# Optimization experiments

Hardware: AMD Instinct MI355X
Metric: run time of the kernel (lower is better)

Reference implementation:

```python
import jax, jax.numpy as jnp
import numpy as np

B, W = 131072, 32
N_SCEN, SDIM = 19, 16
EMBED_DIM, COMP_DIM = 768, 64
INPUT_DIM = EMBED_DIM + N_SCEN * SDIM  # 1072


def setup_inputs() -> dict:
    key = jax.random.key(0)
    k1, k2, k3, k4, k5, k6 = jax.random.split(key, 6)
    intent_embedding = jax.random.normal(k1, (B, EMBED_DIM), dtype=jnp.float32)
    scenario_ids = jax.random.randint(k2, (B, W), 0, N_SCEN, dtype=jnp.int32)
    # Prefix mask: the torch loop iterates the first int(mask.sum()) slots,
    # so the mask must be a contiguous run of ones.
    lengths = jax.random.randint(k3, (B,), 1, W + 1)
    scenario_mask = (jnp.arange(W)[None, :] < lengths[:, None]).astype(jnp.float32)
    # Parameters (init: normal std=0.01, zero biases)
    scenario_table = 0.01 * jax.random.normal(k4, (N_SCEN, SDIM), dtype=jnp.float32)
    W1 = 0.01 * jax.random.normal(k5, (INPUT_DIM, COMP_DIM), dtype=jnp.float32)
    b1 = jnp.zeros((COMP_DIM,), dtype=jnp.float32)
    W2 = 0.01 * jax.random.normal(k6, (COMP_DIM, 1), dtype=jnp.float32)
    b2 = jnp.zeros((1,), dtype=jnp.float32)
    return {
        "intent_embedding": intent_embedding,
        "scenario_ids": scenario_ids,
        "scenario_mask": scenario_mask,
        "scenario_table": scenario_table,
        "W1": W1, "b1": b1, "W2": W2, "b2": b2,
    }


def reference(intent_embedding, scenario_ids, scenario_mask, scenario_table, W1, b1, W2, b2):
    # Embedding lookup: [B, W, SDIM]
    embeds = scenario_table[scenario_ids]
    masked = embeds * scenario_mask[:, :, None]
    # Vectorized scatter-add into per-scenario bins: [B, N_SCEN, SDIM]
    batch_idx = jnp.arange(scenario_ids.shape[0])[:, None]
    bag3 = jnp.zeros(
        (scenario_ids.shape[0], N_SCEN, SDIM), dtype=embeds.dtype
    ).at[batch_idx, scenario_ids].add(masked)
    counts = scenario_mask.sum(axis=1, keepdims=True)
    bag_vec = bag3.reshape(scenario_ids.shape[0], N_SCEN * SDIM) / jnp.maximum(counts, 1.0)
    combined = jnp.concatenate([intent_embedding, bag_vec], axis=1)  # [B, 1072]
    h = jax.nn.relu(combined @ W1 + b1)  # dropout is identity in eval mode
    return jnp.tanh(h @ W2 + b2)  # [B, 1]
```

## Files before the change

kernel.cpp:

```cpp
#include <hip/hip_runtime.h>
#include <hip/hip_bf16.h>
#include <math.h>

using short8 = __attribute__((ext_vector_type(8))) short;
using f32x4  = __attribute__((ext_vector_type(4))) float;
using fv4    = __attribute__((ext_vector_type(4))) float;

#define EMB 768
#define CD  64
#define NSCEN 19
#define KSTEPS 24
#define NCHUNKS (25 * 4)
#define QB 14336
#define BM 128

__device__ __forceinline__ ushort f2bf(float x) {
    unsigned u = __float_as_uint(x);
    u += 0x7FFFu + ((u >> 16) & 1u);
    return (ushort)(u >> 16);
}

__device__ __forceinline__ uint cvt2(float x, float y) {
    __hip_bfloat162 h = __float22bfloat162_rn(make_float2(x, y));
    union { __hip_bfloat162 h; uint u; } c;
    c.h = h;
    return c.u;
}

__global__ void prep_W1T(const float* __restrict__ table,
                         const float* __restrict__ W1,
                         ushort* __restrict__ W1T) {
    int e0 = (blockIdx.x * 256 + threadIdx.x) * 4;
    if (e0 >= NCHUNKS * 512) return;
    int chunk = e0 >> 9, r = e0 & 511;
    int lane = r >> 3, j0 = r & 7;
    int ks = chunk >> 2, ct = chunk & 3;
    int col = ct * 16 + (lane & 15);
    int kbase = ks * 32 + ((lane >> 4) << 3) + j0;
    ushort res[4];
#pragma unroll
    for (int q = 0; q < 4; ++q) {
        int k = kbase + q;
        float v = 0.f;
        if (k < EMB) {
            v = W1[(size_t)k * CD + col];
        } else {
            int s = k - EMB;
            if (s < NSCEN) {
#pragma unroll
                for (int d = 0; d < 16; ++d)
                    v += table[s * 16 + d] * W1[(size_t)(EMB + s * 16 + d) * CD + col];
            }
        }
        res[q] = f2bf(v);
    }
    *(ushort4*)&W1T[e0] = make_ushort4(res[0], res[1], res[2], res[3]);
}

__global__ __launch_bounds__(512, 4)
void scorer_mfma(const float* __restrict__ emb,
                 const int* __restrict__ ids,
                 const float* __restrict__ mask,
                 const ushort* __restrict__ W1T,
                 const float* __restrict__ b1,
                 const float* __restrict__ W2,
                 const float* __restrict__ b2,
                 float* __restrict__ out) {
    __shared__ __align__(16) ushort Bq[2][QB];
    __shared__ __align__(16) ushort bagb[8][16][32];

    const int t    = threadIdx.x;
    const int w    = t >> 6;
    const int lane = t & 63;
    const int lr   = lane & 15;
    const int lg   = lane >> 4;
    const int row0 = blockIdx.x * BM;

    const int hrow = row0 + w * 16 + lr;
    const int*   idrow = ids  + (size_t)hrow * 32 + lg * 8;
    const float* mrow  = mask + (size_t)hrow * 32 + lg * 8;
    int4   iv0 = ((const int4*)idrow)[0],  iv1 = ((const int4*)idrow)[1];
    float4 mv0 = ((const float4*)mrow)[0], mv1 = ((const float4*)mrow)[1];

    const float* ap = emb + (size_t)(row0 + w * 16 + lr) * EMB + (lg << 3);
    fv4 aA[2], aB[2];
#define LOADA(dst, kks) do {                                   \
    const float* _p = ap + (kks) * 32;                         \
    dst[0] = *(const fv4*)(_p);                                \
    dst[1] = *(const fv4*)(_p + 4);                            \
} while (0)
    LOADA(aA, 0);

    uint4 f0, f1, f2, f3;
#define ISSUE_FILL(qs) do {                                                  \
    const uint* _g = (const uint*)((const char*)W1T + (size_t)(qs) * 4096);  \
    f0 = *(const uint4*)(_g + (t)        * 4);                               \
    f1 = *(const uint4*)(_g + (t + 512)  * 4);                               \
    f2 = *(const uint4*)(_g + (t + 1024) * 4);                               \
    if (t < 256) f3 = *(const uint4*)(_g + (t + 1536) * 4);                  \
} while (0)
#define WRITE_FILL(bufi) do {                                                \
    uint* _l = (uint*)&Bq[bufi][0];                                          \
    *(uint4*)(_l + (t)        * 4) = f0;                                     \
    *(uint4*)(_l + (t + 512)  * 4) = f1;                                     \
    *(uint4*)(_l + (t + 1024) * 4) = f2;                                     \
    if (t < 256) *(uint4*)(_l + (t + 1536) * 4) = f3;                        \
} while (0)
    ISSUE_FILL(0);

    float bin[NSCEN];
#pragma unroll
    for (int s = 0; s < NSCEN; ++s) bin[s] = 0.f;
    float cnt = 0.f;
#define HSLOT(idv, mvv) do {                                   \
    cnt += mvv;                                                \
    _Pragma("unroll")                                          \
    for (int s = 0; s < NSCEN; ++s)                            \
        bin[s] += (idv == s) ? mvv : 0.f;                      \
} while (0)
    HSLOT(iv0.x, mv0.x); HSLOT(iv0.y, mv0.y); HSLOT(iv0.z, mv0.z); HSLOT(iv0.w, mv0.w);
    HSLOT(iv1.x, mv1.x); HSLOT(iv1.y, mv1.y); HSLOT(iv1.z, mv1.z); HSLOT(iv1.w, mv1.w);
#undef HSLOT
    cnt += __shfl_xor(cnt, 16);
    cnt += __shfl_xor(cnt, 32);
#pragma unroll
    for (int s = 0; s < NSCEN; ++s) {
        bin[s] += __shfl_xor(bin[s], 16);
        bin[s] += __shfl_xor(bin[s], 32);
    }
    {
        float rc = 1.0f / fmaxf(cnt, 1.0f);
        if (lane < 16) {
            uint u[16];
#pragma unroll
            for (int p = 0; p < 9; ++p) u[p] = cvt2(bin[2 * p] * rc, bin[2 * p + 1] * rc);
            u[9] = cvt2(bin[18] * rc, 0.f);
#pragma unroll
            for (int p = 10; p < 16; ++p) u[p] = 0u;
            ushort* bp = &bagb[w][lane][0];
#pragma unroll
            for (int q = 0; q < 4; ++q)
                *(uint4*)(bp + q * 8) = make_uint4(u[4 * q], u[4 * q + 1], u[4 * q + 2], u[4 * q + 3]);
        }
    }

    WRITE_FILL(0);
    ISSUE_FILL(6);
    __syncthreads();

    f32x4 acc[4];
#pragma unroll
    for (int j = 0; j < 4; ++j) acc[j] = (f32x4)0.f;

    short8 bqr[4];
#define LDSB(bufi, ksl) do {                                   \
    const ushort* _l = &Bq[bufi][(ksl) * 2048 + lane * 8];     \
    bqr[0] = *(const short8*)(_l);                             \
    bqr[1] = *(const short8*)(_l + 512);                       \
    bqr[2] = *(const short8*)(_l + 1024);                      \
    bqr[3] = *(const short8*)(_l + 1536);                      \
} while (0)

#define STEP(areg) do {                                                     \
    union { uint u[4]; short8 s; } _c;                                      \
    _c.u[0] = cvt2(areg[0][0], areg[0][1]);                                 \
    _c.u[1] = cvt2(areg[0][2], areg[0][3]);                                 \
    _c.u[2] = cvt2(areg[1][0], areg[1][1]);                                 \
    _c.u[3] = cvt2(areg[1][2], areg[1][3]);                                 \
    acc[0] = __builtin_amdgcn_mfma_f32_16x16x32_bf16(_c.s, bqr[0], acc[0], 0, 0, 0); \
    acc[1] = __builtin_amdgcn_mfma_f32_16x16x32_bf16(_c.s, bqr[1], acc[1], 0, 0, 0); \
    acc[2] = __builtin_amdgcn_mfma_f32_16x16x32_bf16(_c.s, bqr[2], acc[2], 0, 0, 0); \
    acc[3] = __builtin_amdgcn_mfma_f32_16x16x32_bf16(_c.s, bqr[3], acc[3], 0, 0, 0); \
} while (0)

#define QUARTER(bufi, qs) do {                                              \
    _Pragma("unroll")                                                       \
    for (int _ksl = 0; _ksl < 6; ++_ksl) {                                  \
        const int _ks = (qs) + _ksl;                                        \
        LDSB(bufi, _ksl);                                                   \
        if ((_ks & 1) == 0) {                                               \
            if (_ks + 1 <= 23) LOADA(aB, _ks + 1);                          \
            STEP(aA);                                                       \
        } else {                                                            \
            if (_ks + 1 <= 23) LOADA(aA, _ks + 1);                          \
            STEP(aB);                                                       \
        }                                                                   \
    }                                                                       \
} while (0)

    WRITE_FILL(1);
    ISSUE_FILL(12);
    QUARTER(0, 0);
    __syncthreads();

    WRITE_FILL(0);
    ISSUE_FILL(18);
    QUARTER(1, 6);
    __syncthreads();

    WRITE_FILL(1);
    QUARTER(0, 12);
    __syncthreads();

    QUARTER(1, 18);
    {
        short8 ab = *(const short8*)&bagb[w][lr][lg << 3];
        LDSB(1, 6);
        acc[0] = __builtin_amdgcn_mfma_f32_16x16x32_bf16(ab, bqr[0], acc[0], 0, 0, 0);
        acc[1] = __builtin_amdgcn_mfma_f32_16x16x32_bf16(ab, bqr[1], acc[1], 0, 0, 0);
        acc[2] = __builtin_amdgcn_mfma_f32_16x16x32_bf16(ab, bqr[2], acc[2], 0, 0, 0);
        acc[3] = __builtin_amdgcn_mfma_f32_16x16x32_bf16(ab, bqr[3], acc[3], 0, 0, 0);
    }

    float b1v[4], w2v[4];
#pragma unroll
    for (int ct = 0; ct < 4; ++ct) {
        int c = ct * 16 + lr;
        b1v[ct] = b1[c];
        w2v[ct] = W2[c];
    }
    const float b2v = b2[0];
#pragma unroll
    for (int r = 0; r < 4; ++r) {
        float p = 0.f;
#pragma unroll
        for (int ct = 0; ct < 4; ++ct) {
            float h = acc[ct][r] + b1v[ct];
            p += fmaxf(h, 0.f) * w2v[ct];
        }
        p += __shfl_xor(p, 1);
        p += __shfl_xor(p, 2);
        p += __shfl_xor(p, 4);
        p += __shfl_xor(p, 8);
        if (lr == 0)
            out[row0 + w * 16 + (lg << 2) + r] = tanhf(p + b2v);
    }
#undef ISSUE_FILL
#undef WRITE_FILL
#undef LOADA
#undef LDSB
#undef STEP
#undef QUARTER
}

extern "C" void kernel_launch(void* const* d_in, const int* in_sizes, int n_in,
                              void* d_out, int out_size, void* d_ws, size_t ws_size,
                              hipStream_t stream) {
    const float* emb   = (const float*)d_in[0];
    const int*   ids   = (const int*)d_in[1];
    const float* mask  = (const float*)d_in[2];
    const float* table = (const float*)d_in[3];
    const float* W1    = (const float*)d_in[4];
    const float* b1    = (const float*)d_in[5];
    const float* W2    = (const float*)d_in[6];
    const float* b2    = (const float*)d_in[7];
    float* out  = (float*)d_out;
    ushort* W1T = (ushort*)d_ws;

    prep_W1T<<<50, 256, 0, stream>>>(table, W1, W1T);
    const int nblocks = out_size / BM;
    scorer_mfma<<<nblocks, 512, 0, stream>>>(emb, ids, mask, W1T, b1, W2, b2, out);
}
```

Baseline: 90.28 us.

## Shrink LDS weight staging to 4-kstep groups and raise occupancy to 6 blocks

```diff
diff --git a/kernel.cpp b/kernel.cpp
--- a/kernel.cpp
+++ b/kernel.cpp
@@ -11,7 +11,7 @@
 #define NSCEN 19
 #define KSTEPS 24
 #define NCHUNKS (25 * 4)
-#define QB 14336
+#define GB 8192
 #define BM 128
 
 __device__ __forceinline__ ushort f2bf(float x) {
@@ -57,7 +57,7 @@
     *(ushort4*)&W1T[e0] = make_ushort4(res[0], res[1], res[2], res[3]);
 }
 
-__global__ __launch_bounds__(512, 4)
+__global__ __launch_bounds__(512, 6)
 void scorer_mfma(const float* __restrict__ emb,
                  const int* __restrict__ ids,
                  const float* __restrict__ mask,
@@ -66,7 +66,8 @@
                  const float* __restrict__ W2,
                  const float* __restrict__ b2,
                  float* __restrict__ out) {
-    __shared__ __align__(16) ushort Bq[2][QB];
+    __shared__ __align__(16) ushort Bq[2][GB];
+    __shared__ __align__(16) ushort Pb[2048];
     __shared__ __align__(16) ushort bagb[8][16][32];
 
     const int t    = threadIdx.x;
@@ -91,22 +92,20 @@
 } while (0)
     LOADA(aA, 0);
 
-    uint4 f0, f1, f2, f3;
-#define ISSUE_FILL(qs) do {                                                  \
-    const uint* _g = (const uint*)((const char*)W1T + (size_t)(qs) * 4096);  \
-    f0 = *(const uint4*)(_g + (t)        * 4);                               \
-    f1 = *(const uint4*)(_g + (t + 512)  * 4);                               \
-    f2 = *(const uint4*)(_g + (t + 1024) * 4);                               \
-    if (t < 256) f3 = *(const uint4*)(_g + (t + 1536) * 4);                  \
+    uint4 fA, fB;
+#define ISSUE_FILL(g) do {                                                    \
+    const uint* _g = (const uint*)((const char*)W1T + (size_t)(g) * 16384);  \
+    fA = *(const uint4*)(_g + (t)       * 4);                                \
+    fB = *(const uint4*)(_g + (t + 512) * 4);                                \
 } while (0)
 #define WRITE_FILL(bufi) do {                                                \
     uint* _l = (uint*)&Bq[bufi][0];                                          \
-    *(uint4*)(_l + (t)        * 4) = f0;                                     \
-    *(uint4*)(_l + (t + 512)  * 4) = f1;                                     \
-    *(uint4*)(_l + (t + 1024) * 4) = f2;                                     \
-    if (t < 256) *(uint4*)(_l + (t + 1536) * 4) = f3;                        \
+    *(uint4*)(_l + (t)       * 4) = fA;                                      \
+    *(uint4*)(_l + (t + 512) * 4) = fB;                                      \
 } while (0)
     ISSUE_FILL(0);
+    uint4 pv;
+    if (t < 256) pv = *(const uint4*)((const char*)W1T + 98304 + t * 16);
 
     float bin[NSCEN];
 #pragma unroll
@@ -145,7 +144,8 @@
     }
 
     WRITE_FILL(0);
-    ISSUE_FILL(6);
+    if (t < 256) *(uint4*)((char*)Pb + t * 16) = pv;
+    ISSUE_FILL(1);
     __syncthreads();
 
     f32x4 acc[4];
@@ -173,9 +173,9 @@
     acc[3] = __builtin_amdgcn_mfma_f32_16x16x32_bf16(_c.s, bqr[3], acc[3], 0, 0, 0); \
 } while (0)
 
-#define QUARTER(bufi, qs) do {                                              \
+#define GROUP(bufi, qs) do {                                                \
     _Pragma("unroll")                                                       \
-    for (int _ksl = 0; _ksl < 6; ++_ksl) {                                  \
+    for (int _ksl = 0; _ksl < 4; ++_ksl) {                                  \
         const int _ks = (qs) + _ksl;                                        \
         LDSB(bufi, _ksl);                                                   \
         if ((_ks & 1) == 0) {                                               \
@@ -188,28 +188,38 @@
     }                                                                       \
 } while (0)
 
+    WRITE_FILL(1); ISSUE_FILL(2);
+    GROUP(0, 0);
+    __syncthreads();
+
+    WRITE_FILL(0); ISSUE_FILL(3);
+    GROUP(1, 4);
+    __syncthreads();
+
+    WRITE_FILL(1); ISSUE_FILL(4);
+    GROUP(0, 8);
+    __syncthreads();
+
+    WRITE_FILL(0); ISSUE_FILL(5);
+    GROUP(1, 12);
+    __syncthreads();
+
     WRITE_FILL(1);
-    ISSUE_FILL(12);
-    QUARTER(0, 0);
-    __syncthreads();
-
-    WRITE_FILL(0);
-    ISSUE_FILL(18);
-    QUARTER(1, 6);
-    __syncthreads();
-
-    WRITE_FILL(1);
-    QUARTER(0, 12);
-    __syncthreads();
-
-    QUARTER(1, 18);
+    GROUP(0, 16);
+    __syncthreads();
+
+    GROUP(1, 20);
     {
         short8 ab = *(const short8*)&bagb[w][lr][lg << 3];
-        LDSB(1, 6);
-        acc[0] = __builtin_amdgcn_mfma_f32_16x16x32_bf16(ab, bqr[0], acc[0], 0, 0, 0);
-        acc[1] = __builtin_amdgcn_mfma_f32_16x16x32_bf16(ab, bqr[1], acc[1], 0, 0, 0);
-        acc[2] = __builtin_amdgcn_mfma_f32_16x16x32_bf16(ab, bqr[2], acc[2], 0, 0, 0);
-        acc[3] = __builtin_amdgcn_mfma_f32_16x16x32_bf16(ab, bqr[3], acc[3], 0, 0, 0);
+        const ushort* _l = &Pb[lane * 8];
+        short8 p0 = *(const short8*)(_l);
+        short8 p1 = *(const short8*)(_l + 512);
+        short8 p2 = *(const short8*)(_l + 1024);
+        short8 p3 = *(const short8*)(_l + 1536);
+        acc[0] = __builtin_amdgcn_mfma_f32_16x16x32_bf16(ab, p0, acc[0], 0, 0, 0);
+        acc[1] = __builtin_amdgcn_mfma_f32_16x16x32_bf16(ab, p1, acc[1], 0, 0, 0);
+        acc[2] = __builtin_amdgcn_mfma_f32_16x16x32_bf16(ab, p2, acc[2], 0, 0, 0);
+        acc[3] = __builtin_amdgcn_mfma_f32_16x16x32_bf16(ab, p3, acc[3], 0, 0, 0);
     }
 
     float b1v[4], w2v[4];
@@ -240,7 +250,7 @@
 #undef LOADA
 #undef LDSB
 #undef STEP
-#undef QUARTER
+#undef GROUP
 }
 
 extern "C" void kernel_launch(void* const* d_in, const int* in_sizes, int n_in,
```

Result: no change. 90.34 us (+0.1%).
